# Optimization experiments

Hardware: AMD Instinct MI355X
Metric: run time of the kernel (lower is better)

The kernel has to match this reference:

```python
import jax, jax.numpy as jnp
import numpy as np
import math

B, N, D = 16, 2048, 256

def setup_inputs() -> dict:
    key = jax.random.key(0)
    kq, kk, kv = jax.random.split(key, 3)
    query = jax.random.normal(kq, (B, N, D), dtype=jnp.float32)
    k = jax.random.normal(kk, (B, N, D), dtype=jnp.float32)
    value = jax.random.normal(kv, (B, D, N), dtype=jnp.float32)  # channel-first [B, d_v, N]
    return {"query": query, "key": k, "value": value, "mask": 0}

def reference(query, key, value, mask):
    d_k = query.shape[-1]
    scale = 1.0 / math.sqrt(d_k)
    # scores: [B, N, N]
    scores = jnp.einsum('bnd,bmd->bnm', query, key) * scale
    p_attn = jax.nn.softmax(scores, axis=-1)
    # mask is a static Python int flag gating dropout; mask=0 -> no dropout (deterministic reference)
    if mask:
        pass  # dropout intentionally disabled in deterministic reference
    # out = p_attn @ value^T  -> [B, N, d_v]; module returns out.transpose(-2,-1) -> [B, d_v, N]
    out_t = jnp.einsum('bnm,bdm->bdn', p_attn, value)
    return (out_t, p_attn)
```

## Files before the change

### kernel.cpp

```cpp
#include <hip/hip_runtime.h>
#include <hip/hip_bf16.h>


using bf16x8 = __attribute__((ext_vector_type(8))) short;
using f32x4  = __attribute__((ext_vector_type(4))) float;

__device__ __forceinline__ short f2bf(float f) {
    unsigned u = __float_as_uint(f);
    u += 0x7fffu + ((u >> 16) & 1u);
    return (short)(u >> 16);
}

__device__ __forceinline__ f32x4 mfma16(bf16x8 a, bf16x8 b, f32x4 c) {
    return __builtin_amdgcn_mfma_f32_16x16x32_bf16(a, b, c, 0, 0, 0);
}

#define AS1(p) ((const __attribute__((address_space(1))) void*)(p))
#define AS3(p) ((__attribute__((address_space(3))) void*)(p))

__global__ __launch_bounds__(256)
void convert_qkv(const float* __restrict__ Q, const float* __restrict__ K,
                 const float* __restrict__ V, short* __restrict__ Qb,
                 short* __restrict__ Kb, short* __restrict__ Vb, size_t n8)
{
    size_t i = (size_t)blockIdx.x * 256 + threadIdx.x;
    const float* src;
    short* dst;
    float scale = 1.0f;
    if (i < n8)            { src = Q;  dst = Qb; scale = 0.0625f; }
    else if (i < 2 * n8)   { i -= n8;      src = K; dst = Kb; }
    else                   { i -= 2 * n8;  src = V; dst = Vb; }
    const f32x4* s4 = (const f32x4*)src;
    f32x4 a = __builtin_nontemporal_load(s4 + i * 2);
    f32x4 b = __builtin_nontemporal_load(s4 + i * 2 + 1);
    bf16x8 v;
    v[0] = f2bf(a[0] * scale); v[1] = f2bf(a[1] * scale);
    v[2] = f2bf(a[2] * scale); v[3] = f2bf(a[3] * scale);
    v[4] = f2bf(b[0] * scale); v[5] = f2bf(b[1] * scale);
    v[6] = f2bf(b[2] * scale); v[7] = f2bf(b[3] * scale);
    *(bf16x8*)(dst + i * 8) = v;
}

__global__ __launch_bounds__(512, 2)
void fused_attn(const short* __restrict__ Qb, const short* __restrict__ Kb,
                const short* __restrict__ Vb, float* __restrict__ Pout,
                float* __restrict__ outT)
{
    __shared__ __align__(16) short Klds[2][64 * 256];
    __shared__ __align__(16) short Vlds[2][256 * 64];
    __shared__ __align__(16) short Plds[128 * 64];
    __shared__ float lpart[8][32];

    constexpr float LOG2E = 1.4426950408889634f;

    const unsigned g  = blockIdx.x;
    const unsigned wg = (g & 7) * 32 + (g >> 3);
    const int b  = (int)(wg >> 4);
    const int nb = (int)(wg & 15);

    const int tid  = threadIdx.x;
    const int lane = tid & 63;
    const int wave = tid >> 6;
    const int wn  = wave >> 1;
    const int wm  = wave & 1;
    const int l15 = lane & 15;
    const int l4  = lane >> 4;

    const short* Kbase = Kb + (size_t)b * (2048 * 256);
    const short* Vbase = Vb + (size_t)b * (256 * 2048);

    const short* Qp = Qb + ((size_t)b * 2048 + (size_t)nb * 128) * 256;
    bf16x8 qf[2][8];
#pragma unroll
    for (int mf = 0; mf < 2; mf++)
#pragma unroll
        for (int ks = 0; ks < 8; ks++)
            qf[mf][ks] = *(const bf16x8*)(
                Qp + (size_t)(wn * 32 + mf * 16 + l15) * 256 + ks * 32 + l4 * 8);

    auto stage_k = [&](int t, int buf) {
#pragma unroll
        for (int i = 0; i < 4; i++) {
            int ml = i * 16 + wave * 2 + (lane >> 5);
            int c  = lane & 31;
            int cs = (c & 24) | ((c ^ ml) & 7);
            __builtin_amdgcn_global_load_lds(
                AS1(Kbase + (size_t)(t * 64 + ml) * 256 + cs * 8),
                AS3(&Klds[buf][i * 4096 + wave * 512]), 16, 0, 0);
        }
    };
    auto stage_v = [&](int t, int buf) {
#pragma unroll
        for (int i = 0; i < 4; i++) {
            int d  = i * 64 + wave * 8 + (lane >> 3);
            int c  = lane & 7;
            int cs = c ^ (d & 7);
            __builtin_amdgcn_global_load_lds(
                AS1(Vbase + (size_t)d * 2048 + t * 64 + cs * 8),
                AS3(&Vlds[buf][i * 4096 + wave * 512]), 16, 0, 0);
        }
    };

    auto qkt = [&](int buf, f32x4 sac[2][2]) {
#pragma unroll
        for (int ks = 0; ks < 8; ks++) {
            bf16x8 kf[2];
#pragma unroll
            for (int nf = 0; nf < 2; nf++) {
                int m  = wm * 32 + nf * 16 + l15;
                int ch = (ks * 4 + l4) ^ (m & 7);
                kf[nf] = *(const bf16x8*)((const char*)&Klds[buf][0] + m * 512 + ch * 16);
            }
#pragma unroll
            for (int mf = 0; mf < 2; mf++)
#pragma unroll
                for (int nf = 0; nf < 2; nf++)
                    sac[mf][nf] = mfma16(qf[mf][ks], kf[nf], sac[mf][nf]);
        }
    };

    float lacc[2][4] = {{0.f, 0.f, 0.f, 0.f}, {0.f, 0.f, 0.f, 0.f}};
    stage_k(0, 0);
    for (int t = 0; t < 32; t++) {
        __syncthreads();
        if (t + 1 < 32) stage_k(t + 1, (t + 1) & 1);
        f32x4 sac[2][2];
#pragma unroll
        for (int mf = 0; mf < 2; mf++)
#pragma unroll
            for (int nf = 0; nf < 2; nf++)
                sac[mf][nf] = f32x4{0.f, 0.f, 0.f, 0.f};
        qkt(t & 1, sac);
#pragma unroll
        for (int mf = 0; mf < 2; mf++)
#pragma unroll
            for (int nf = 0; nf < 2; nf++)
#pragma unroll
                for (int r = 0; r < 4; r++)
                    lacc[mf][r] += exp2f(sac[mf][nf][r] * LOG2E);
    }
#pragma unroll
    for (int dlt = 1; dlt < 16; dlt <<= 1)
#pragma unroll
        for (int mf = 0; mf < 2; mf++)
#pragma unroll
            for (int r = 0; r < 4; r++)
                lacc[mf][r] += __shfl_xor(lacc[mf][r], dlt);
    if (l15 == 0)
#pragma unroll
        for (int mf = 0; mf < 2; mf++)
#pragma unroll
            for (int r = 0; r < 4; r++)
                lpart[wave][mf * 16 + l4 * 4 + r] = lacc[mf][r];
    __syncthreads();
    float rl[2][4];
#pragma unroll
    for (int mf = 0; mf < 2; mf++)
#pragma unroll
        for (int r = 0; r < 4; r++) {
            int row = mf * 16 + l4 * 4 + r;
            rl[mf][r] = 1.0f / (lpart[wn * 2 + 0][row] + lpart[wn * 2 + 1][row]);
        }

    f32x4 oac[4][4];
#pragma unroll
    for (int i = 0; i < 4; i++)
#pragma unroll
        for (int j = 0; j < 4; j++)
            oac[i][j] = f32x4{0.f, 0.f, 0.f, 0.f};

    stage_k(0, 0);
    stage_v(0, 0);
    float* prow = Pout + ((size_t)b * 2048 + (size_t)nb * 128) * 2048;

    for (int t = 0; t < 32; t++) {
        __syncthreads();
        if (t + 1 < 32) { stage_k(t + 1, (t + 1) & 1); stage_v(t + 1, (t + 1) & 1); }

        f32x4 sac[2][2];
#pragma unroll
        for (int mf = 0; mf < 2; mf++)
#pragma unroll
            for (int nf = 0; nf < 2; nf++)
                sac[mf][nf] = f32x4{0.f, 0.f, 0.f, 0.f};
        qkt(t & 1, sac);

        float pv[2][2][4];
#pragma unroll
        for (int mf = 0; mf < 2; mf++)
#pragma unroll
            for (int nf = 0; nf < 2; nf++)
#pragma unroll
                for (int r = 0; r < 4; r++) {
                    pv[mf][nf][r] = exp2f(sac[mf][nf][r] * LOG2E) * rl[mf][r];
                    int n = wn * 32 + mf * 16 + l4 * 4 + r;
                    int m = wm * 32 + nf * 16 + l15;
                    int byte = n * 128 + ((((m >> 3) ^ (n & 7))) << 4) + (m & 7) * 2;
                    *(short*)((char*)Plds + byte) = f2bf(pv[mf][nf][r]);
                }
        __syncthreads();

        const char* vb_ = (const char*)&Vlds[t & 1][0];
#pragma unroll
        for (int ksl = 0; ksl < 2; ksl++) {
            bf16x8 vf[4], pf[4];
#pragma unroll
            for (int mf4 = 0; mf4 < 4; mf4++) {
                int d  = wn * 64 + mf4 * 16 + l15;
                int ch = (ksl * 4 + l4) ^ (d & 7);
                vf[mf4] = *(const bf16x8*)(vb_ + d * 128 + ch * 16);
            }
#pragma unroll
            for (int nf4 = 0; nf4 < 4; nf4++) {
                int n  = wm * 64 + nf4 * 16 + l15;
                int ch = (ksl * 4 + l4) ^ (n & 7);
                pf[nf4] = *(const bf16x8*)((const char*)Plds + n * 128 + ch * 16);
            }
#pragma unroll
            for (int mf4 = 0; mf4 < 4; mf4++)
#pragma unroll
                for (int nf4 = 0; nf4 < 4; nf4++)
                    oac[mf4][nf4] = mfma16(vf[mf4], pf[nf4], oac[mf4][nf4]);
        }

        const int m0 = t * 64;
#pragma unroll
        for (int mf = 0; mf < 2; mf++)
#pragma unroll
            for (int nf = 0; nf < 2; nf++)
#pragma unroll
                for (int r = 0; r < 4; r++) {
                    int n = wn * 32 + mf * 16 + l4 * 4 + r;
                    int m = m0 + wm * 32 + nf * 16 + l15;
                    __builtin_nontemporal_store(pv[mf][nf][r],
                                                prow + (size_t)n * 2048 + m);
                }
    }

    float* op = outT + (size_t)b * (256 * 2048) + (size_t)nb * 128;
#pragma unroll
    for (int mf4 = 0; mf4 < 4; mf4++)
#pragma unroll
        for (int nf4 = 0; nf4 < 4; nf4++)
#pragma unroll
            for (int r = 0; r < 4; r++) {
                int d = wn * 64 + mf4 * 16 + l4 * 4 + r;
                int n = wm * 64 + nf4 * 16 + l15;
                op[(size_t)d * 2048 + n] = oac[mf4][nf4][r];
            }
}

template<int BM, int BN, int BK>
__global__ __launch_bounds__(256)
void gemm_abt(const float* __restrict__ A, const float* __restrict__ B,
              float* __restrict__ C, int M, int N, int K,
              long strideA, long strideB, long strideC, float scale)
{
    const int b  = blockIdx.z;
    const int bm = blockIdx.y;
    const int bn = blockIdx.x;
    A += (size_t)b * strideA;
    B += (size_t)b * strideB;
    C += (size_t)b * strideC;

    constexpr int LDT = BK + 8;
    __shared__ __align__(16) short Alds[BM][LDT];
    __shared__ __align__(16) short Blds[BN][LDT];

    const int tid  = threadIdx.x;
    const int lane = tid & 63;
    const int wave = tid >> 6;
    const int wr   = wave >> 1;
    const int wc   = wave & 1;

    f32x4 acc[4][4];
#pragma unroll
    for (int m = 0; m < 4; m++)
#pragma unroll
        for (int n = 0; n < 4; n++)
            acc[m][n] = f32x4{0.f, 0.f, 0.f, 0.f};

    const float* Ab = A + (size_t)(bm * BM) * K;
    const float* Bb = B + (size_t)(bn * BN) * K;

    const int tr  = tid >> 4;
    const int tc4 = (tid & 15) << 2;

    for (int k0 = 0; k0 < K; k0 += BK) {
        __syncthreads();
#pragma unroll
        for (int r = tr; r < BM; r += 16) {
            const float4 v = *(const float4*)(Ab + (size_t)r * K + k0 + tc4);
            short4 s;
            s.x = f2bf(v.x); s.y = f2bf(v.y); s.z = f2bf(v.z); s.w = f2bf(v.w);
            *(short4*)&Alds[r][tc4] = s;
        }
#pragma unroll
        for (int r = tr; r < BN; r += 16) {
            const float4 v = *(const float4*)(Bb + (size_t)r * K + k0 + tc4);
            short4 s;
            s.x = f2bf(v.x); s.y = f2bf(v.y); s.z = f2bf(v.z); s.w = f2bf(v.w);
            *(short4*)&Blds[r][tc4] = s;
        }
        __syncthreads();

#pragma unroll
        for (int kk = 0; kk < BK; kk += 32) {
            const int ko = kk + ((lane >> 4) << 3);
            bf16x8 af[4], bfr[4];
#pragma unroll
            for (int m = 0; m < 4; m++)
                af[m] = *(const bf16x8*)&Alds[wr * 64 + m * 16 + (lane & 15)][ko];
#pragma unroll
            for (int n = 0; n < 4; n++)
                bfr[n] = *(const bf16x8*)&Blds[wc * 64 + n * 16 + (lane & 15)][ko];
#pragma unroll
            for (int m = 0; m < 4; m++)
#pragma unroll
                for (int n = 0; n < 4; n++)
                    acc[m][n] = __builtin_amdgcn_mfma_f32_16x16x32_bf16(
                        af[m], bfr[n], acc[m][n], 0, 0, 0);
        }
    }

    float* Cb = C + (size_t)(bm * BM) * N + (size_t)bn * BN;
    const int rbase = wr * 64 + ((lane >> 4) << 2);
    const int cbase = wc * 64 + (lane & 15);
#pragma unroll
    for (int m = 0; m < 4; m++)
#pragma unroll
        for (int n = 0; n < 4; n++)
#pragma unroll
            for (int r = 0; r < 4; r++)
                Cb[(size_t)(rbase + m * 16 + r) * N + cbase + n * 16] =
                    acc[m][n][r] * scale;
}

__global__ __launch_bounds__(256)
void softmax_rows(float* __restrict__ P)
{
    const size_t row = blockIdx.x;
    float* p = P + row * 2048;
    const int tid  = threadIdx.x;
    const int lane = tid & 63;
    const int wave = tid >> 6;

    float4 v0 = ((const float4*)p)[tid];
    float4 v1 = ((const float4*)p)[tid + 256];

    float m = fmaxf(fmaxf(fmaxf(v0.x, v0.y), fmaxf(v0.z, v0.w)),
                    fmaxf(fmaxf(v1.x, v1.y), fmaxf(v1.z, v1.w)));
#pragma unroll
    for (int off = 32; off; off >>= 1) m = fmaxf(m, __shfl_xor(m, off));

    __shared__ float sred[4];
    __shared__ float ssum[4];
    if (lane == 0) sred[wave] = m;
    __syncthreads();
    m = fmaxf(fmaxf(sred[0], sred[1]), fmaxf(sred[2], sred[3]));

    v0.x = expf(v0.x - m); v0.y = expf(v0.y - m);
    v0.z = expf(v0.z - m); v0.w = expf(v0.w - m);
    v1.x = expf(v1.x - m); v1.y = expf(v1.y - m);
    v1.z = expf(v1.z - m); v1.w = expf(v1.w - m);

    float s = (v0.x + v0.y + v0.z + v0.w) + (v1.x + v1.y + v1.z + v1.w);
#pragma unroll
    for (int off = 32; off; off >>= 1) s += __shfl_xor(s, off);
    if (lane == 0) ssum[wave] = s;
    __syncthreads();
    s = ssum[0] + ssum[1] + ssum[2] + ssum[3];

    const float r = 1.0f / s;
    v0.x *= r; v0.y *= r; v0.z *= r; v0.w *= r;
    v1.x *= r; v1.y *= r; v1.z *= r; v1.w *= r;

    ((float4*)p)[tid]       = v0;
    ((float4*)p)[tid + 256] = v1;
}

extern "C" void kernel_launch(void* const* d_in, const int* in_sizes, int n_in,
                              void* d_out, int out_size, void* d_ws, size_t ws_size,
                              hipStream_t stream)
{
    const float* Q  = (const float*)d_in[0];
    const float* Kk = (const float*)d_in[1];
    const float* V  = (const float*)d_in[2];

    float* outT = (float*)d_out;
    float* P    = outT + (size_t)16 * 256 * 2048;

    const size_t nQ = (size_t)16 * 2048 * 256;
    const long sQK = (long)2048 * 256;
    const long sP  = (long)2048 * 2048;
    const long sO  = (long)256 * 2048;

    const size_t needQKV = 3 * nQ * sizeof(short);

    if (ws_size >= needQKV) {
        short* Qb = (short*)d_ws;
        short* Kb = Qb + nQ;
        short* Vb = Kb + nQ;

        convert_qkv<<<dim3((unsigned)(3 * nQ / 8 / 256)), 256, 0, stream>>>(
            Q, Kk, V, Qb, Kb, Vb, nQ / 8);

        fused_attn<<<dim3(256), 512, 0, stream>>>(Qb, Kb, Vb, P, outT);
    } else {
        gemm_abt<128, 128, 64><<<dim3(16, 16, 16), 256, 0, stream>>>(
            Q, Kk, P, 2048, 2048, 256, sQK, sQK, sP, 0.0625f);
        softmax_rows<<<dim3(16 * 2048), 256, 0, stream>>>(P);
        gemm_abt<128, 128, 64><<<dim3(16, 2, 16), 256, 0, stream>>>(
            V, P, outT, 256, 2048, 2048, sO, sP, sO, 1.0f);
    }
}
```

Measured before the change: 195.8 us.

## Transpose QK^T MFMA, vectorize P stores, drop V LDS staging, raise occupancy

Swaps the MFMA operand order so each lane holds four consecutive key columns of one query row. This allows 16-byte vectorized nontemporal stores of P and short4 writes into the P LDS tile. The V tile is no longer staged in LDS and is read directly from global memory, and lpart now aliases the P buffer. Together these cut LDS use so launch bounds can request 4 blocks per SM. The risks are uncoalesced, uncached-pattern global V reads and tighter register limits that could spill the 64-float output accumulator.

```diff
diff --git a/kernel.cpp b/kernel.cpp
--- a/kernel.cpp
+++ b/kernel.cpp
@@ -41,15 +41,14 @@
     *(bf16x8*)(dst + i * 8) = v;
 }
 
-__global__ __launch_bounds__(512, 2)
+__global__ __launch_bounds__(512, 4)
 void fused_attn(const short* __restrict__ Qb, const short* __restrict__ Kb,
                 const short* __restrict__ Vb, float* __restrict__ Pout,
                 float* __restrict__ outT)
 {
     __shared__ __align__(16) short Klds[2][64 * 256];
-    __shared__ __align__(16) short Vlds[2][256 * 64];
     __shared__ __align__(16) short Plds[128 * 64];
-    __shared__ float lpart[8][32];
+    float* lpart = (float*)Plds;
 
     constexpr float LOG2E = 1.4426950408889634f;
 
@@ -89,19 +88,8 @@
                 AS3(&Klds[buf][i * 4096 + wave * 512]), 16, 0, 0);
         }
     };
-    auto stage_v = [&](int t, int buf) {
-#pragma unroll
-        for (int i = 0; i < 4; i++) {
-            int d  = i * 64 + wave * 8 + (lane >> 3);
-            int c  = lane & 7;
-            int cs = c ^ (d & 7);
-            __builtin_amdgcn_global_load_lds(
-                AS1(Vbase + (size_t)d * 2048 + t * 64 + cs * 8),
-                AS3(&Vlds[buf][i * 4096 + wave * 512]), 16, 0, 0);
-        }
-    };
-
-    auto qkt = [&](int buf, f32x4 sac[2][2]) {
+
+    auto qkt = [&](int buf, f32x4 sacT[2][2]) {
 #pragma unroll
         for (int ks = 0; ks < 8; ks++) {
             bf16x8 kf[2];
@@ -115,52 +103,45 @@
             for (int mf = 0; mf < 2; mf++)
 #pragma unroll
                 for (int nf = 0; nf < 2; nf++)
-                    sac[mf][nf] = mfma16(qf[mf][ks], kf[nf], sac[mf][nf]);
+                    sacT[mf][nf] = mfma16(kf[nf], qf[mf][ks], sacT[mf][nf]);
         }
     };
 
-    float lacc[2][4] = {{0.f, 0.f, 0.f, 0.f}, {0.f, 0.f, 0.f, 0.f}};
+    float lacc[2] = {0.f, 0.f};
     stage_k(0, 0);
     for (int t = 0; t < 32; t++) {
         __syncthreads();
         if (t + 1 < 32) stage_k(t + 1, (t + 1) & 1);
-        f32x4 sac[2][2];
+        f32x4 sacT[2][2];
 #pragma unroll
         for (int mf = 0; mf < 2; mf++)
 #pragma unroll
             for (int nf = 0; nf < 2; nf++)
-                sac[mf][nf] = f32x4{0.f, 0.f, 0.f, 0.f};
-        qkt(t & 1, sac);
+                sacT[mf][nf] = f32x4{0.f, 0.f, 0.f, 0.f};
+        qkt(t & 1, sacT);
 #pragma unroll
         for (int mf = 0; mf < 2; mf++)
 #pragma unroll
             for (int nf = 0; nf < 2; nf++)
 #pragma unroll
                 for (int r = 0; r < 4; r++)
-                    lacc[mf][r] += exp2f(sac[mf][nf][r] * LOG2E);
-    }
-#pragma unroll
-    for (int dlt = 1; dlt < 16; dlt <<= 1)
-#pragma unroll
-        for (int mf = 0; mf < 2; mf++)
-#pragma unroll
-            for (int r = 0; r < 4; r++)
-                lacc[mf][r] += __shfl_xor(lacc[mf][r], dlt);
-    if (l15 == 0)
-#pragma unroll
-        for (int mf = 0; mf < 2; mf++)
-#pragma unroll
-            for (int r = 0; r < 4; r++)
-                lpart[wave][mf * 16 + l4 * 4 + r] = lacc[mf][r];
+                    lacc[mf] += exp2f(sacT[mf][nf][r] * LOG2E);
+    }
+#pragma unroll
+    for (int mf = 0; mf < 2; mf++) {
+        lacc[mf] += __shfl_xor(lacc[mf], 16);
+        lacc[mf] += __shfl_xor(lacc[mf], 32);
+    }
+    if (l4 == 0) {
+        lpart[wave * 32 + 0 * 16 + l15] = lacc[0];
+        lpart[wave * 32 + 1 * 16 + l15] = lacc[1];
+    }
     __syncthreads();
-    float rl[2][4];
+    float rl[2];
 #pragma unroll
     for (int mf = 0; mf < 2; mf++)
-#pragma unroll
-        for (int r = 0; r < 4; r++) {
-            int row = mf * 16 + l4 * 4 + r;
-            rl[mf][r] = 1.0f / (lpart[wn * 2 + 0][row] + lpart[wn * 2 + 1][row]);
-        }
+        rl[mf] = 1.0f / (lpart[(wn * 2 + 0) * 32 + mf * 16 + l15] +
+                         lpart[(wn * 2 + 1) * 32 + mf * 16 + l15]);
 
     f32x4 oac[4][4];
 #pragma unroll
@@ -170,50 +151,61 @@
             oac[i][j] = f32x4{0.f, 0.f, 0.f, 0.f};
 
     stage_k(0, 0);
-    stage_v(0, 0);
     float* prow = Pout + ((size_t)b * 2048 + (size_t)nb * 128) * 2048;
 
     for (int t = 0; t < 32; t++) {
         __syncthreads();
-        if (t + 1 < 32) { stage_k(t + 1, (t + 1) & 1); stage_v(t + 1, (t + 1) & 1); }
-
-        f32x4 sac[2][2];
+        f32x4 sacT[2][2];
 #pragma unroll
         for (int mf = 0; mf < 2; mf++)
 #pragma unroll
             for (int nf = 0; nf < 2; nf++)
-                sac[mf][nf] = f32x4{0.f, 0.f, 0.f, 0.f};
-        qkt(t & 1, sac);
-
-        float pv[2][2][4];
-#pragma unroll
-        for (int mf = 0; mf < 2; mf++)
-#pragma unroll
-            for (int nf = 0; nf < 2; nf++)
-#pragma unroll
-                for (int r = 0; r < 4; r++) {
-                    pv[mf][nf][r] = exp2f(sac[mf][nf][r] * LOG2E) * rl[mf][r];
-                    int n = wn * 32 + mf * 16 + l4 * 4 + r;
-                    int m = wm * 32 + nf * 16 + l15;
-                    int byte = n * 128 + ((((m >> 3) ^ (n & 7))) << 4) + (m & 7) * 2;
-                    *(short*)((char*)Plds + byte) = f2bf(pv[mf][nf][r]);
-                }
-        __syncthreads();
-
-        const char* vb_ = (const char*)&Vlds[t & 1][0];
+                sacT[mf][nf] = f32x4{0.f, 0.f, 0.f, 0.f};
+        qkt(t & 1, sacT);
+
+        f32x4 pv4[2][2];
+#pragma unroll
+        for (int mf = 0; mf < 2; mf++)
+#pragma unroll
+            for (int nf = 0; nf < 2; nf++) {
+#pragma unroll
+                for (int r = 0; r < 4; r++)
+                    pv4[mf][nf][r] = exp2f(sacT[mf][nf][r] * LOG2E) * rl[mf];
+                short4 ps;
+                ps.x = f2bf(pv4[mf][nf][0]); ps.y = f2bf(pv4[mf][nf][1]);
+                ps.z = f2bf(pv4[mf][nf][2]); ps.w = f2bf(pv4[mf][nf][3]);
+                const int n  = wn * 32 + mf * 16 + l15;
+                const int mb = wm * 32 + nf * 16 + l4 * 4;
+                const int ch = (mb >> 3) ^ (n & 7);
+                *(short4*)((char*)Plds + n * 128 + ch * 16 + (mb & 7) * 2) = ps;
+            }
+        __syncthreads();
+
+        if (t + 1 < 32) stage_k(t + 1, (t + 1) & 1);
+
+#pragma unroll
+        for (int mf = 0; mf < 2; mf++)
+#pragma unroll
+            for (int nf = 0; nf < 2; nf++) {
+                const int n  = wn * 32 + mf * 16 + l15;
+                const int m  = t * 64 + wm * 32 + nf * 16 + l4 * 4;
+                __builtin_nontemporal_store(pv4[mf][nf],
+                    (f32x4*)(prow + (size_t)n * 2048 + m));
+            }
+
 #pragma unroll
         for (int ksl = 0; ksl < 2; ksl++) {
             bf16x8 vf[4], pf[4];
 #pragma unroll
             for (int mf4 = 0; mf4 < 4; mf4++) {
-                int d  = wn * 64 + mf4 * 16 + l15;
-                int ch = (ksl * 4 + l4) ^ (d & 7);
-                vf[mf4] = *(const bf16x8*)(vb_ + d * 128 + ch * 16);
+                const int d = wn * 64 + mf4 * 16 + l15;
+                vf[mf4] = *(const bf16x8*)(
+                    Vbase + (size_t)d * 2048 + t * 64 + ksl * 32 + l4 * 8);
             }
 #pragma unroll
             for (int nf4 = 0; nf4 < 4; nf4++) {
-                int n  = wm * 64 + nf4 * 16 + l15;
-                int ch = (ksl * 4 + l4) ^ (n & 7);
+                const int n  = wm * 64 + nf4 * 16 + l15;
+                const int ch = (ksl * 4 + l4) ^ (n & 7);
                 pf[nf4] = *(const bf16x8*)((const char*)Plds + n * 128 + ch * 16);
             }
 #pragma unroll
@@ -222,19 +214,6 @@
                 for (int nf4 = 0; nf4 < 4; nf4++)
                     oac[mf4][nf4] = mfma16(vf[mf4], pf[nf4], oac[mf4][nf4]);
         }
-
-        const int m0 = t * 64;
-#pragma unroll
-        for (int mf = 0; mf < 2; mf++)
-#pragma unroll
-            for (int nf = 0; nf < 2; nf++)
-#pragma unroll
-                for (int r = 0; r < 4; r++) {
-                    int n = wn * 32 + mf * 16 + l4 * 4 + r;
-                    int m = m0 + wm * 32 + nf * 16 + l15;
-                    __builtin_nontemporal_store(pv[mf][nf][r],
-                                                prow + (size_t)n * 2048 + m);
-                }
     }
 
     float* op = outT + (size_t)b * (256 * 2048) + (size_t)nb * 128;
```

Result: slower. 462.3 us (+136.1%).
